# Kernel tuning notes

Measured on AMD Instinct MI355X. Metric: run time of the kernel, lower is better.

The kernel has to match this reference:

```python
import jax, jax.numpy as jnp
from jax import lax
import numpy as np

P, C, D, K, N = 16, 48, 32, 4, 262144
GRID = (512, 512, 128)
MAT_MODE = ((0, 1), (0, 2), (1, 2))


def setup_inputs() -> dict:
    key = jax.random.key(0)
    ks = jax.random.split(key, 9)
    pts = jax.random.uniform(ks[0], (1, N, 3), jnp.float32, -1.0, 1.0)
    topk_id = jax.random.randint(ks[1], (K,), 0, P)
    w = jax.random.uniform(ks[2], (K,), jnp.float32)
    topk_weight = w / jnp.sum(w)  # F.normalize(p=1)
    line0 = 0.1 * jax.random.normal(ks[3], (P, C, GRID[0]), jnp.float32)
    line1 = 0.1 * jax.random.normal(ks[4], (P, C, GRID[1]), jnp.float32)
    line2 = 0.1 * jax.random.normal(ks[5], (P, C, GRID[2]), jnp.float32)
    feat0 = 0.1 * jax.random.normal(ks[6], (P, C, D), jnp.float32)
    feat1 = 0.1 * jax.random.normal(ks[7], (P, C, D), jnp.float32)
    feat2 = 0.1 * jax.random.normal(ks[8], (P, C, D), jnp.float32)
    return dict(pts=pts, topk_id=topk_id, topk_weight=topk_weight,
                line0=line0, line1=line1, line2=line2,
                feat0=feat0, feat1=feat1, feat2=feat2)


def _interp_line(line, coords):
    # 1D linear interpolation (grid_sample with x=0, align_corners=True).
    # line: [K, C, G], coords: [n] in [-1, 1] -> [K, C, n]
    G = line.shape[-1]
    pos = (coords + 1.0) * 0.5 * (G - 1)
    i0 = jnp.clip(jnp.floor(pos), 0, G - 2).astype(jnp.int32)
    w = (pos - i0.astype(pos.dtype))  # [n]
    v0 = line[:, :, i0]       # gather -> [K, C, n]
    v1 = line[:, :, i0 + 1]
    return v0 * (1.0 - w) + v1 * w


def reference(pts, topk_id, topk_weight, line0, line1, line2, feat0, feat1, feat2):
    # pts is detached in the original (normalize_pts calls pts.detach())
    p = lax.stop_gradient(pts).reshape(-1, 3)  # [n, 3]
    lines = (line0[topk_id], line1[topk_id], line2[topk_id])   # [K, C, G_i]
    feats = (feat0[topk_id], feat1[topk_id], feat2[topk_id])   # [K, C, D]
    coord = [_interp_line(lines[i], p[:, i]) for i in range(3)]
    planes = [
        jnp.einsum('kcn,kcd->knd', coord[a] * coord[b], feats[i])
        for i, (a, b) in enumerate(MAT_MODE)
    ]
    pose_feats = jnp.concatenate(planes, axis=-1)           # [K, n, 3D]
    pose_feat = jnp.einsum('k,knd->nd', topk_weight, pose_feats)[None]  # [1, n, 96]
    return pose_feat
```

## Files before the change

### kernel.cpp

```cpp
#include <hip/hip_runtime.h>
#include <hip/hip_fp16.h>

typedef float f4 __attribute__((ext_vector_type(4)));
typedef float f32x4 __attribute__((ext_vector_type(4)));
typedef _Float16 f16x8 __attribute__((ext_vector_type(8)));
typedef unsigned int u32x4 __attribute__((ext_vector_type(4)));

#define NPTS 262144
#define CDIM 48
#define DDIM 32
#define KDIM 4
#define G0 512
#define G1 512
#define G2 128

#define TPB_TILES 4

#define T0_OFF 18432
#define T1_OFF (18432 + 98304)
#define T2_OFF (18432 + 2 * 98304)

static __forceinline__ __device__ unsigned short f2h(float f) {
    _Float16 h = (_Float16)f;
    return __builtin_bit_cast(unsigned short, h);
}
static __forceinline__ __device__ __half2 h2(unsigned int u) {
    return __builtin_bit_cast(__half2, u);
}
static __forceinline__ __device__ unsigned int h2u(__half2 h) {
    return __builtin_bit_cast(unsigned int, h);
}

__global__ void pack_kernel(const int* __restrict__ topk_id,
                            const float* __restrict__ tw,
                            const float* __restrict__ line0,
                            const float* __restrict__ line1,
                            const float* __restrict__ line2,
                            const float* __restrict__ feat0,
                            const float* __restrict__ feat1,
                            const float* __restrict__ feat2,
                            unsigned short* __restrict__ ws) {
    int tid = blockIdx.x * blockDim.x + threadIdx.x;
    int stride = gridDim.x * blockDim.x;

    for (int idx = tid; idx < 3 * 2 * 6 * 64 * 8; idx += stride) {
        int j = idx & 7;
        int l = (idx >> 3) & 63;
        int kt = (idx >> 9) % 6;
        int t = (idx / 3072) % 2;
        int i = idx / 6144;
        int kc = kt * 32 + (l >> 4) * 8 + j;
        int k = kc / 48;
        int c = kc - k * 48;
        int d = t * 16 + (l & 15);
        const float* f = (i == 0) ? feat0 : (i == 1) ? feat1 : feat2;
        float val = tw[k] * f[((size_t)topk_id[k] * CDIM + c) * DDIM + d];
        ws[idx] = f2h(val);
    }
    for (int idx = tid; idx < KDIM * G0 * CDIM; idx += stride) {
        int c = idx % CDIM;
        int g = (idx / CDIM) % G0;
        int k = idx / (CDIM * G0);
        int src = (topk_id[k] * CDIM + c) * G0 + g;
        ws[T0_OFF + idx] = f2h(line0[src]);
        ws[T1_OFF + idx] = f2h(line1[src]);
    }
    for (int idx = tid; idx < KDIM * G2 * CDIM; idx += stride) {
        int c = idx % CDIM;
        int g = (idx / CDIM) % G2;
        int k = idx / (CDIM * G2);
        ws[T2_OFF + idx] = f2h(line2[(topk_id[k] * CDIM + c) * G2 + g]);
    }
}

__global__ __launch_bounds__(256, 2) void main_kernel(const float* __restrict__ pts,
                                                      const unsigned short* __restrict__ ws,
                                                      float* __restrict__ out) {
    __shared__ __align__(16) unsigned short sWB[18432];

    const int lane = threadIdx.x & 63;
    const int wave = threadIdx.x >> 6;
    const int row = lane & 15;
    const int h = lane >> 4;

    float P0x, P0y, P0z, P1x, P1y, P1z, P2x, P2y, P2z, P3x, P3y, P3z;
    {
        const int pb = blockIdx.x * TPB_TILES * 64 + wave * 16 + row;
        P0x = pts[(pb + 0 * 64) * 3 + 0]; P0y = pts[(pb + 0 * 64) * 3 + 1]; P0z = pts[(pb + 0 * 64) * 3 + 2];
        P1x = pts[(pb + 1 * 64) * 3 + 0]; P1y = pts[(pb + 1 * 64) * 3 + 1]; P1z = pts[(pb + 1 * 64) * 3 + 2];
        P2x = pts[(pb + 2 * 64) * 3 + 0]; P2y = pts[(pb + 2 * 64) * 3 + 1]; P2z = pts[(pb + 2 * 64) * 3 + 2];
        P3x = pts[(pb + 3 * 64) * 3 + 0]; P3y = pts[(pb + 3 * 64) * 3 + 1]; P3z = pts[(pb + 3 * 64) * 3 + 2];
    }
    asm volatile("" : "+v"(P0x), "+v"(P0y), "+v"(P0z), "+v"(P1x), "+v"(P1y), "+v"(P1z),
                      "+v"(P2x), "+v"(P2y), "+v"(P2z), "+v"(P3x), "+v"(P3y), "+v"(P3z));

    {
        const u32x4* src = (const u32x4*)ws;
        u32x4* dst = (u32x4*)sWB;
        for (int i = threadIdx.x; i < 2304; i += 256) dst[i] = src[i];
    }
    __syncthreads();

    const unsigned short* T0 = ws + T0_OFF;
    const unsigned short* T1 = ws + T1_OFF;
    const unsigned short* T2 = ws + T2_OFF;
    const u32x4* wb = (const u32x4*)sWB;

#pragma unroll
    for (int tile = 0; tile < TPB_TILES; ++tile) {
        const int base = (blockIdx.x * TPB_TILES + tile) * 64 + wave * 16;

        const float px = (tile == 0) ? P0x : (tile == 1) ? P1x : (tile == 2) ? P2x : P3x;
        const float py = (tile == 0) ? P0y : (tile == 1) ? P1y : (tile == 2) ? P2y : P3y;
        const float pz = (tile == 0) ? P0z : (tile == 1) ? P1z : (tile == 2) ? P2z : P3z;

        float pos0 = (px + 1.0f) * (0.5f * (float)(G0 - 1));
        int i00 = min(max((int)floorf(pos0), 0), G0 - 2);
        float w0 = pos0 - (float)i00;

        float pos1 = (py + 1.0f) * (0.5f * (float)(G1 - 1));
        int i01 = min(max((int)floorf(pos1), 0), G1 - 2);
        float w1 = pos1 - (float)i01;

        float pos2 = (pz + 1.0f) * (0.5f * (float)(G2 - 1));
        int i02 = min(max((int)floorf(pos2), 0), G2 - 2);
        float w2 = pos2 - (float)i02;

        const __half2 W0 = __float2half2_rn(w0), OM0 = __float2half2_rn(1.0f - w0);
        const __half2 W1 = __float2half2_rn(w1), OM1 = __float2half2_rn(1.0f - w1);
        const __half2 W2 = __float2half2_rn(w2), OM2 = __float2half2_rn(1.0f - w2);

        f32x4 acc00 = {0.f, 0.f, 0.f, 0.f}, acc01 = acc00;
        f32x4 acc10 = acc00, acc11 = acc00;
        f32x4 acc20 = acc00, acc21 = acc00;

#define DECL_LD(n) u32x4 n##a0, n##b0, n##a1, n##b1, n##a2, n##b2
#define LOADKT(n, KT) {                                                        \
        int kc_ = (KT) * 32 + h * 8;                                           \
        int k_ = kc_ / 48;                                                     \
        int c_ = kc_ - k_ * 48;                                                \
        const unsigned short* t0_ = T0 + (k_ * G0 + i00) * CDIM + c_;          \
        const unsigned short* t1_ = T1 + (k_ * G1 + i01) * CDIM + c_;          \
        const unsigned short* t2_ = T2 + (k_ * G2 + i02) * CDIM + c_;          \
        n##a0 = *(const u32x4*)t0_;  n##b0 = *(const u32x4*)(t0_ + CDIM);      \
        n##a1 = *(const u32x4*)t1_;  n##b1 = *(const u32x4*)(t1_ + CDIM);      \
        n##a2 = *(const u32x4*)t2_;  n##b2 = *(const u32x4*)(t2_ + CDIM); }
#define KEEP36()                                                               \
    asm volatile("" : "+v"(q0a0), "+v"(q0b0), "+v"(q0a1), "+v"(q0b1),          \
                      "+v"(q0a2), "+v"(q0b2),                                  \
                      "+v"(q1a0), "+v"(q1b0), "+v"(q1a1), "+v"(q1b1),          \
                      "+v"(q1a2), "+v"(q1b2),                                  \
                      "+v"(q2a0), "+v"(q2b0), "+v"(q2a1), "+v"(q2b1),          \
                      "+v"(q2a2), "+v"(q2b2),                                  \
                      "+v"(q3a0), "+v"(q3b0), "+v"(q3a1), "+v"(q3b1),          \
                      "+v"(q3a2), "+v"(q3b2),                                  \
                      "+v"(q4a0), "+v"(q4b0), "+v"(q4a1), "+v"(q4b1),          \
                      "+v"(q4a2), "+v"(q4b2),                                  \
                      "+v"(q5a0), "+v"(q5b0), "+v"(q5a1), "+v"(q5b1),          \
                      "+v"(q5a2), "+v"(q5b2))
#define COMPUTEKT(n, KT) {                                                     \
        u32x4 pa01, pa02, pa12;                                                \
        _Pragma("unroll")                                                      \
        for (int j = 0; j < 4; ++j) {                                          \
            __half2 x0 = __hfma2(h2(n##b0[j]), W0, __hmul2(h2(n##a0[j]), OM0));\
            __half2 x1 = __hfma2(h2(n##b1[j]), W1, __hmul2(h2(n##a1[j]), OM1));\
            __half2 x2 = __hfma2(h2(n##b2[j]), W2, __hmul2(h2(n##a2[j]), OM2));\
            pa01[j] = h2u(__hmul2(x0, x1));                                    \
            pa02[j] = h2u(__hmul2(x0, x2));                                    \
            pa12[j] = h2u(__hmul2(x1, x2));                                    \
        }                                                                      \
        f16x8 fa01 = __builtin_bit_cast(f16x8, pa01);                          \
        f16x8 fa02 = __builtin_bit_cast(f16x8, pa02);                          \
        f16x8 fa12 = __builtin_bit_cast(f16x8, pa12);                          \
        acc00 = __builtin_amdgcn_mfma_f32_16x16x32_f16(__builtin_bit_cast(f16x8, wb[(0 * 6 + (KT)) * 64 + lane]), fa01, acc00, 0, 0, 0); \
        acc01 = __builtin_amdgcn_mfma_f32_16x16x32_f16(__builtin_bit_cast(f16x8, wb[(1 * 6 + (KT)) * 64 + lane]), fa01, acc01, 0, 0, 0); \
        acc10 = __builtin_amdgcn_mfma_f32_16x16x32_f16(__builtin_bit_cast(f16x8, wb[(2 * 6 + (KT)) * 64 + lane]), fa02, acc10, 0, 0, 0); \
        acc11 = __builtin_amdgcn_mfma_f32_16x16x32_f16(__builtin_bit_cast(f16x8, wb[(3 * 6 + (KT)) * 64 + lane]), fa02, acc11, 0, 0, 0); \
        acc20 = __builtin_amdgcn_mfma_f32_16x16x32_f16(__builtin_bit_cast(f16x8, wb[(4 * 6 + (KT)) * 64 + lane]), fa12, acc20, 0, 0, 0); \
        acc21 = __builtin_amdgcn_mfma_f32_16x16x32_f16(__builtin_bit_cast(f16x8, wb[(5 * 6 + (KT)) * 64 + lane]), fa12, acc21, 0, 0, 0); }

        DECL_LD(q0); DECL_LD(q1); DECL_LD(q2);
        DECL_LD(q3); DECL_LD(q4); DECL_LD(q5);

        LOADKT(q0, 0); LOADKT(q1, 1); LOADKT(q2, 2);
        LOADKT(q3, 3); LOADKT(q4, 4); LOADKT(q5, 5);
        KEEP36();

        COMPUTEKT(q0, 0);
        COMPUTEKT(q1, 1);
        COMPUTEKT(q2, 2);
        COMPUTEKT(q3, 3);
        COMPUTEKT(q4, 4);
        COMPUTEKT(q5, 5);

#undef DECL_LD
#undef LOADKT
#undef KEEP36
#undef COMPUTEKT

        {
            float* o = out + (size_t)(base + row) * 96 + h * 4;
            *(f4*)(o + 0)  = acc00;
            *(f4*)(o + 16) = acc01;
            *(f4*)(o + 32) = acc10;
            *(f4*)(o + 48) = acc11;
            *(f4*)(o + 64) = acc20;
            *(f4*)(o + 80) = acc21;
        }
    }
}

extern "C" void kernel_launch(void* const* d_in, const int* in_sizes, int n_in,
                              void* d_out, int out_size, void* d_ws, size_t ws_size,
                              hipStream_t stream) {
    const float* pts = (const float*)d_in[0];
    const int* topk_id = (const int*)d_in[1];
    const float* tw = (const float*)d_in[2];
    const float* line0 = (const float*)d_in[3];
    const float* line1 = (const float*)d_in[4];
    const float* line2 = (const float*)d_in[5];
    const float* feat0 = (const float*)d_in[6];
    const float* feat1 = (const float*)d_in[7];
    const float* feat2 = (const float*)d_in[8];
    float* out = (float*)d_out;
    unsigned short* ws = (unsigned short*)d_ws;

    pack_kernel<<<512, 256, 0, stream>>>(topk_id, tw, line0, line1, line2,
                                         feat0, feat1, feat2, ws);
    main_kernel<<<NPTS / (64 * TPB_TILES), 256, 0, stream>>>(pts, ws, out);
}
```

Baseline: 70.23 us.

## Sort points by z/x grid cell via counting sort to improve gather locality

Adds histogram, single-block scan, and scatter kernels that build a permutation grouping points by their (z-cell, x-cell) bucket, then has the main kernel process points in that order and write outputs scattered back to original indices. The aim is better cache locality for the line-table gathers, whose rows are scattered across random coordinates. In exchange it adds three extra launches, global atomics on a 65536-entry counter array, a serial single-block scan, an indirect point load, and non-contiguous output stores.

```diff
diff --git a/kernel.cpp b/kernel.cpp
--- a/kernel.cpp
+++ b/kernel.cpp
@@ -19,6 +19,10 @@
 #define T0_OFF 18432
 #define T1_OFF (18432 + 98304)
 #define T2_OFF (18432 + 2 * 98304)
+#define PERM_OFF 119808
+#define RANK_OFF 381952
+#define CNT_OFF 644096
+#define NBUCKET 65536
 
 static __forceinline__ __device__ unsigned short f2h(float f) {
     _Float16 h = (_Float16)f;
@@ -29,6 +33,14 @@
 }
 static __forceinline__ __device__ unsigned int h2u(__half2 h) {
     return __builtin_bit_cast(unsigned int, h);
+}
+static __forceinline__ __device__ int cell0(float x) {
+    float pos = (x + 1.0f) * (0.5f * (float)(G0 - 1));
+    return min(max((int)floorf(pos), 0), G0 - 2);
+}
+static __forceinline__ __device__ int cell2(float z) {
+    float pos = (z + 1.0f) * (0.5f * (float)(G2 - 1));
+    return min(max((int)floorf(pos), 0), G2 - 2);
 }
 
 __global__ void pack_kernel(const int* __restrict__ topk_id,
@@ -42,6 +54,9 @@
                             unsigned short* __restrict__ ws) {
     int tid = blockIdx.x * blockDim.x + threadIdx.x;
     int stride = gridDim.x * blockDim.x;
+    unsigned int* cnt = (unsigned int*)ws + CNT_OFF;
+
+    for (int idx = tid; idx < NBUCKET; idx += stride) cnt[idx] = 0;
 
     for (int idx = tid; idx < 3 * 2 * 6 * 64 * 8; idx += stride) {
         int j = idx & 7;
@@ -54,8 +69,7 @@
         int c = kc - k * 48;
         int d = t * 16 + (l & 15);
         const float* f = (i == 0) ? feat0 : (i == 1) ? feat1 : feat2;
-        float val = tw[k] * f[((size_t)topk_id[k] * CDIM + c) * DDIM + d];
-        ws[idx] = f2h(val);
+        ws[idx] = f2h(tw[k] * f[((size_t)topk_id[k] * CDIM + c) * DDIM + d]);
     }
     for (int idx = tid; idx < KDIM * G0 * CDIM; idx += stride) {
         int c = idx % CDIM;
@@ -73,6 +87,47 @@
     }
 }
 
+__global__ void hist_kernel(const float* __restrict__ pts, unsigned int* __restrict__ wsu) {
+    int n = blockIdx.x * blockDim.x + threadIdx.x;
+    if (n >= NPTS) return;
+    int key = (cell2(pts[n * 3 + 2]) << 9) | cell0(pts[n * 3 + 0]);
+    wsu[RANK_OFF + n] = atomicAdd(&wsu[CNT_OFF + key], 1u);
+}
+
+__global__ void scan_kernel(unsigned int* __restrict__ wsu) {
+    __shared__ unsigned int sa[1024], sb[1024];
+    unsigned int* counts = wsu + CNT_OFF;
+    int t = threadIdx.x;
+    unsigned int s = 0;
+    for (int i = 0; i < 64; ++i) s += counts[t * 64 + i];
+    sa[t] = s;
+    __syncthreads();
+    unsigned int* src = sa;
+    unsigned int* dst = sb;
+    for (int off = 1; off < 1024; off <<= 1) {
+        unsigned int v = src[t];
+        if (t >= off) v += src[t - off];
+        __syncthreads();
+        dst[t] = v;
+        __syncthreads();
+        unsigned int* tmp = src; src = dst; dst = tmp;
+    }
+    unsigned int run = (t == 0) ? 0u : src[t - 1];
+    for (int i = 0; i < 64; ++i) {
+        unsigned int c = counts[t * 64 + i];
+        counts[t * 64 + i] = run;
+        run += c;
+    }
+}
+
+__global__ void scatter_kernel(const float* __restrict__ pts, unsigned int* __restrict__ wsu) {
+    int n = blockIdx.x * blockDim.x + threadIdx.x;
+    if (n >= NPTS) return;
+    int key = (cell2(pts[n * 3 + 2]) << 9) | cell0(pts[n * 3 + 0]);
+    unsigned int slot = wsu[CNT_OFF + key] + wsu[RANK_OFF + n];
+    wsu[PERM_OFF + slot] = (unsigned int)n;
+}
+
 __global__ __launch_bounds__(256, 2) void main_kernel(const float* __restrict__ pts,
                                                       const unsigned short* __restrict__ ws,
                                                       float* __restrict__ out) {
@@ -82,14 +137,20 @@
     const int wave = threadIdx.x >> 6;
     const int row = lane & 15;
     const int h = lane >> 4;
-
+    const unsigned int* perm = (const unsigned int*)ws + PERM_OFF;
+
+    int n0, n1, n2, n3;
     float P0x, P0y, P0z, P1x, P1y, P1z, P2x, P2y, P2z, P3x, P3y, P3z;
     {
-        const int pb = blockIdx.x * TPB_TILES * 64 + wave * 16 + row;
-        P0x = pts[(pb + 0 * 64) * 3 + 0]; P0y = pts[(pb + 0 * 64) * 3 + 1]; P0z = pts[(pb + 0 * 64) * 3 + 2];
-        P1x = pts[(pb + 1 * 64) * 3 + 0]; P1y = pts[(pb + 1 * 64) * 3 + 1]; P1z = pts[(pb + 1 * 64) * 3 + 2];
-        P2x = pts[(pb + 2 * 64) * 3 + 0]; P2y = pts[(pb + 2 * 64) * 3 + 1]; P2z = pts[(pb + 2 * 64) * 3 + 2];
-        P3x = pts[(pb + 3 * 64) * 3 + 0]; P3y = pts[(pb + 3 * 64) * 3 + 1]; P3z = pts[(pb + 3 * 64) * 3 + 2];
+        const int sb = blockIdx.x * TPB_TILES * 64 + wave * 16 + row;
+        n0 = (int)perm[sb + 0 * 64];
+        n1 = (int)perm[sb + 1 * 64];
+        n2 = (int)perm[sb + 2 * 64];
+        n3 = (int)perm[sb + 3 * 64];
+        P0x = pts[n0 * 3 + 0]; P0y = pts[n0 * 3 + 1]; P0z = pts[n0 * 3 + 2];
+        P1x = pts[n1 * 3 + 0]; P1y = pts[n1 * 3 + 1]; P1z = pts[n1 * 3 + 2];
+        P2x = pts[n2 * 3 + 0]; P2y = pts[n2 * 3 + 1]; P2z = pts[n2 * 3 + 2];
+        P3x = pts[n3 * 3 + 0]; P3y = pts[n3 * 3 + 1]; P3z = pts[n3 * 3 + 2];
     }
     asm volatile("" : "+v"(P0x), "+v"(P0y), "+v"(P0z), "+v"(P1x), "+v"(P1y), "+v"(P1z),
                       "+v"(P2x), "+v"(P2y), "+v"(P2z), "+v"(P3x), "+v"(P3y), "+v"(P3z));
@@ -108,8 +169,7 @@
 
 #pragma unroll
     for (int tile = 0; tile < TPB_TILES; ++tile) {
-        const int base = (blockIdx.x * TPB_TILES + tile) * 64 + wave * 16;
-
+        const int nn = (tile == 0) ? n0 : (tile == 1) ? n1 : (tile == 2) ? n2 : n3;
         const float px = (tile == 0) ? P0x : (tile == 1) ? P1x : (tile == 2) ? P2x : P3x;
         const float py = (tile == 0) ? P0y : (tile == 1) ? P1y : (tile == 2) ? P2y : P3y;
         const float pz = (tile == 0) ? P0z : (tile == 1) ? P1z : (tile == 2) ? P2z : P3z;
@@ -199,7 +259,7 @@
 #undef COMPUTEKT
 
         {
-            float* o = out + (size_t)(base + row) * 96 + h * 4;
+            float* o = out + (size_t)nn * 96 + h * 4;
             *(f4*)(o + 0)  = acc00;
             *(f4*)(o + 16) = acc01;
             *(f4*)(o + 32) = acc10;
@@ -224,8 +284,12 @@
     const float* feat2 = (const float*)d_in[8];
     float* out = (float*)d_out;
     unsigned short* ws = (unsigned short*)d_ws;
+    unsigned int* wsu = (unsigned int*)d_ws;
 
     pack_kernel<<<512, 256, 0, stream>>>(topk_id, tw, line0, line1, line2,
                                          feat0, feat1, feat2, ws);
-    main_kernel<<<NPTS / (64 * TPB_TILES), 256, 0, stream>>>(pts, ws, out);
-}
+    hist_kernel<<<NPTS / 256, 256, 0, stream>>>(pts, wsu);
+    scan_kernel<<<1, 1024, 0, stream>>>(wsu);
+    scatter_kernel<<<NPTS / 256, 256, 0, stream>>>(pts, wsu);
+    main_kernel<<<NPTS / 256, 256, 0, stream>>>(pts, ws, out);
+}
```

After: 106.4 us. +51.4%, slower.

## Double-buffer per-tile gather loads across tiles and overlap with LDS weight staging

Applied to the files above, without the earlier changes.

Restructures the per-block tile loop into a software pipeline with two register sets (q and r). The next tile's 36 gathered table vectors are issued before the current tile's MFMA compute, and the first tile's loads go out before the shared-memory weight copy and barrier. Sched barriers pin this order. The aim is to hide global-load latency behind compute and the LDS fill. The cost is roughly double the load registers, which risks spills or lower occupancy under launch_bounds(256,2).

```diff
diff --git a/kernel.cpp b/kernel.cpp
--- a/kernel.cpp
+++ b/kernel.cpp
@@ -13,8 +13,6 @@
 #define G0 512
 #define G1 512
 #define G2 128
-
-#define TPB_TILES 4
 
 #define T0_OFF 18432
 #define T1_OFF (18432 + 98304)
@@ -54,8 +52,7 @@
         int c = kc - k * 48;
         int d = t * 16 + (l & 15);
         const float* f = (i == 0) ? feat0 : (i == 1) ? feat1 : feat2;
-        float val = tw[k] * f[((size_t)topk_id[k] * CDIM + c) * DDIM + d];
-        ws[idx] = f2h(val);
+        ws[idx] = f2h(tw[k] * f[((size_t)topk_id[k] * CDIM + c) * DDIM + d]);
     }
     for (int idx = tid; idx < KDIM * G0 * CDIM; idx += stride) {
         int c = idx % CDIM;
@@ -82,10 +79,11 @@
     const int wave = threadIdx.x >> 6;
     const int row = lane & 15;
     const int h = lane >> 4;
+    const int blkbase = blockIdx.x * 256 + wave * 16;
 
     float P0x, P0y, P0z, P1x, P1y, P1z, P2x, P2y, P2z, P3x, P3y, P3z;
     {
-        const int pb = blockIdx.x * TPB_TILES * 64 + wave * 16 + row;
+        const int pb = blkbase + row;
         P0x = pts[(pb + 0 * 64) * 3 + 0]; P0y = pts[(pb + 0 * 64) * 3 + 1]; P0z = pts[(pb + 0 * 64) * 3 + 2];
         P1x = pts[(pb + 1 * 64) * 3 + 0]; P1y = pts[(pb + 1 * 64) * 3 + 1]; P1z = pts[(pb + 1 * 64) * 3 + 2];
         P2x = pts[(pb + 2 * 64) * 3 + 0]; P2y = pts[(pb + 2 * 64) * 3 + 1]; P2z = pts[(pb + 2 * 64) * 3 + 2];
@@ -94,70 +92,54 @@
     asm volatile("" : "+v"(P0x), "+v"(P0y), "+v"(P0z), "+v"(P1x), "+v"(P1y), "+v"(P1z),
                       "+v"(P2x), "+v"(P2y), "+v"(P2z), "+v"(P3x), "+v"(P3y), "+v"(P3z));
 
-    {
-        const u32x4* src = (const u32x4*)ws;
-        u32x4* dst = (u32x4*)sWB;
-        for (int i = threadIdx.x; i < 2304; i += 256) dst[i] = src[i];
-    }
-    __syncthreads();
+#define PREP(t, PX, PY, PZ)                                                    \
+    float pos0_##t = (PX + 1.0f) * (0.5f * (float)(G0 - 1));                   \
+    int i00_##t = min(max((int)floorf(pos0_##t), 0), G0 - 2);                  \
+    float w0_##t = pos0_##t - (float)i00_##t;                                  \
+    float pos1_##t = (PY + 1.0f) * (0.5f * (float)(G1 - 1));                   \
+    int i01_##t = min(max((int)floorf(pos1_##t), 0), G1 - 2);                  \
+    float w1_##t = pos1_##t - (float)i01_##t;                                  \
+    float pos2_##t = (PZ + 1.0f) * (0.5f * (float)(G2 - 1));                   \
+    int i02_##t = min(max((int)floorf(pos2_##t), 0), G2 - 2);                  \
+    float w2_##t = pos2_##t - (float)i02_##t;
+
+    PREP(0, P0x, P0y, P0z)
+    PREP(1, P1x, P1y, P1z)
+    PREP(2, P2x, P2y, P2z)
+    PREP(3, P3x, P3y, P3z)
 
     const unsigned short* T0 = ws + T0_OFF;
     const unsigned short* T1 = ws + T1_OFF;
     const unsigned short* T2 = ws + T2_OFF;
-    const u32x4* wb = (const u32x4*)sWB;
-
-#pragma unroll
-    for (int tile = 0; tile < TPB_TILES; ++tile) {
-        const int base = (blockIdx.x * TPB_TILES + tile) * 64 + wave * 16;
-
-        const float px = (tile == 0) ? P0x : (tile == 1) ? P1x : (tile == 2) ? P2x : P3x;
-        const float py = (tile == 0) ? P0y : (tile == 1) ? P1y : (tile == 2) ? P2y : P3y;
-        const float pz = (tile == 0) ? P0z : (tile == 1) ? P1z : (tile == 2) ? P2z : P3z;
-
-        float pos0 = (px + 1.0f) * (0.5f * (float)(G0 - 1));
-        int i00 = min(max((int)floorf(pos0), 0), G0 - 2);
-        float w0 = pos0 - (float)i00;
-
-        float pos1 = (py + 1.0f) * (0.5f * (float)(G1 - 1));
-        int i01 = min(max((int)floorf(pos1), 0), G1 - 2);
-        float w1 = pos1 - (float)i01;
-
-        float pos2 = (pz + 1.0f) * (0.5f * (float)(G2 - 1));
-        int i02 = min(max((int)floorf(pos2), 0), G2 - 2);
-        float w2 = pos2 - (float)i02;
-
-        const __half2 W0 = __float2half2_rn(w0), OM0 = __float2half2_rn(1.0f - w0);
-        const __half2 W1 = __float2half2_rn(w1), OM1 = __float2half2_rn(1.0f - w1);
-        const __half2 W2 = __float2half2_rn(w2), OM2 = __float2half2_rn(1.0f - w2);
-
-        f32x4 acc00 = {0.f, 0.f, 0.f, 0.f}, acc01 = acc00;
-        f32x4 acc10 = acc00, acc11 = acc00;
-        f32x4 acc20 = acc00, acc21 = acc00;
 
 #define DECL_LD(n) u32x4 n##a0, n##b0, n##a1, n##b1, n##a2, n##b2
-#define LOADKT(n, KT) {                                                        \
+#define DECLW(w) DECL_LD(w##0); DECL_LD(w##1); DECL_LD(w##2); \
+                 DECL_LD(w##3); DECL_LD(w##4); DECL_LD(w##5)
+#define LOADKT(n, KT, t) {                                                     \
         int kc_ = (KT) * 32 + h * 8;                                           \
         int k_ = kc_ / 48;                                                     \
         int c_ = kc_ - k_ * 48;                                                \
-        const unsigned short* t0_ = T0 + (k_ * G0 + i00) * CDIM + c_;          \
-        const unsigned short* t1_ = T1 + (k_ * G1 + i01) * CDIM + c_;          \
-        const unsigned short* t2_ = T2 + (k_ * G2 + i02) * CDIM + c_;          \
+        const unsigned short* t0_ = T0 + (k_ * G0 + i00_##t) * CDIM + c_;      \
+        const unsigned short* t1_ = T1 + (k_ * G1 + i01_##t) * CDIM + c_;      \
+        const unsigned short* t2_ = T2 + (k_ * G2 + i02_##t) * CDIM + c_;      \
         n##a0 = *(const u32x4*)t0_;  n##b0 = *(const u32x4*)(t0_ + CDIM);      \
         n##a1 = *(const u32x4*)t1_;  n##b1 = *(const u32x4*)(t1_ + CDIM);      \
         n##a2 = *(const u32x4*)t2_;  n##b2 = *(const u32x4*)(t2_ + CDIM); }
-#define KEEP36()                                                               \
-    asm volatile("" : "+v"(q0a0), "+v"(q0b0), "+v"(q0a1), "+v"(q0b1),          \
-                      "+v"(q0a2), "+v"(q0b2),                                  \
-                      "+v"(q1a0), "+v"(q1b0), "+v"(q1a1), "+v"(q1b1),          \
-                      "+v"(q1a2), "+v"(q1b2),                                  \
-                      "+v"(q2a0), "+v"(q2b0), "+v"(q2a1), "+v"(q2b1),          \
-                      "+v"(q2a2), "+v"(q2b2),                                  \
-                      "+v"(q3a0), "+v"(q3b0), "+v"(q3a1), "+v"(q3b1),          \
-                      "+v"(q3a2), "+v"(q3b2),                                  \
-                      "+v"(q4a0), "+v"(q4b0), "+v"(q4a1), "+v"(q4b1),          \
-                      "+v"(q4a2), "+v"(q4b2),                                  \
-                      "+v"(q5a0), "+v"(q5b0), "+v"(q5a1), "+v"(q5b1),          \
-                      "+v"(q5a2), "+v"(q5b2))
+#define LOAD36(w, t) LOADKT(w##0, 0, t) LOADKT(w##1, 1, t) LOADKT(w##2, 2, t) \
+                     LOADKT(w##3, 3, t) LOADKT(w##4, 4, t) LOADKT(w##5, 5, t)
+#define KEEP36W(p)                                                             \
+    asm volatile("" : "+v"(p##0a0), "+v"(p##0b0), "+v"(p##0a1), "+v"(p##0b1),  \
+                      "+v"(p##0a2), "+v"(p##0b2),                              \
+                      "+v"(p##1a0), "+v"(p##1b0), "+v"(p##1a1), "+v"(p##1b1),  \
+                      "+v"(p##1a2), "+v"(p##1b2),                              \
+                      "+v"(p##2a0), "+v"(p##2b0), "+v"(p##2a1), "+v"(p##2b1),  \
+                      "+v"(p##2a2), "+v"(p##2b2),                              \
+                      "+v"(p##3a0), "+v"(p##3b0), "+v"(p##3a1), "+v"(p##3b1),  \
+                      "+v"(p##3a2), "+v"(p##3b2),                              \
+                      "+v"(p##4a0), "+v"(p##4b0), "+v"(p##4a1), "+v"(p##4b1),  \
+                      "+v"(p##4a2), "+v"(p##4b2),                              \
+                      "+v"(p##5a0), "+v"(p##5b0), "+v"(p##5a1), "+v"(p##5b1),  \
+                      "+v"(p##5a2), "+v"(p##5b2))
 #define COMPUTEKT(n, KT) {                                                     \
         u32x4 pa01, pa02, pa12;                                                \
         _Pragma("unroll")                                                      \
@@ -178,36 +160,62 @@
         acc11 = __builtin_amdgcn_mfma_f32_16x16x32_f16(__builtin_bit_cast(f16x8, wb[(3 * 6 + (KT)) * 64 + lane]), fa02, acc11, 0, 0, 0); \
         acc20 = __builtin_amdgcn_mfma_f32_16x16x32_f16(__builtin_bit_cast(f16x8, wb[(4 * 6 + (KT)) * 64 + lane]), fa12, acc20, 0, 0, 0); \
         acc21 = __builtin_amdgcn_mfma_f32_16x16x32_f16(__builtin_bit_cast(f16x8, wb[(5 * 6 + (KT)) * 64 + lane]), fa12, acc21, 0, 0, 0); }
-
-        DECL_LD(q0); DECL_LD(q1); DECL_LD(q2);
-        DECL_LD(q3); DECL_LD(q4); DECL_LD(q5);
-
-        LOADKT(q0, 0); LOADKT(q1, 1); LOADKT(q2, 2);
-        LOADKT(q3, 3); LOADKT(q4, 4); LOADKT(q5, 5);
-        KEEP36();
-
-        COMPUTEKT(q0, 0);
-        COMPUTEKT(q1, 1);
-        COMPUTEKT(q2, 2);
-        COMPUTEKT(q3, 3);
-        COMPUTEKT(q4, 4);
-        COMPUTEKT(q5, 5);
-
+#define COMPUTE_TILE(w, t) {                                                   \
+        const __half2 W0 = __float2half2_rn(w0_##t), OM0 = __float2half2_rn(1.0f - w0_##t); \
+        const __half2 W1 = __float2half2_rn(w1_##t), OM1 = __float2half2_rn(1.0f - w1_##t); \
+        const __half2 W2 = __float2half2_rn(w2_##t), OM2 = __float2half2_rn(1.0f - w2_##t); \
+        f32x4 acc00 = {0.f, 0.f, 0.f, 0.f}, acc01 = acc00;                     \
+        f32x4 acc10 = acc00, acc11 = acc00;                                    \
+        f32x4 acc20 = acc00, acc21 = acc00;                                    \
+        COMPUTEKT(w##0, 0) COMPUTEKT(w##1, 1) COMPUTEKT(w##2, 2)               \
+        COMPUTEKT(w##3, 3) COMPUTEKT(w##4, 4) COMPUTEKT(w##5, 5)               \
+        float* o = out + (size_t)(blkbase + (t) * 64 + row) * 96 + h * 4;      \
+        *(f4*)(o + 0)  = acc00;                                                \
+        *(f4*)(o + 16) = acc01;                                                \
+        *(f4*)(o + 32) = acc10;                                                \
+        *(f4*)(o + 48) = acc11;                                                \
+        *(f4*)(o + 64) = acc20;                                                \
+        *(f4*)(o + 80) = acc21; }
+
+    DECLW(q); DECLW(r);
+
+    LOAD36(q, 0)
+
+    {
+        const u32x4* src = (const u32x4*)ws;
+        u32x4* dst = (u32x4*)sWB;
+        for (int i = threadIdx.x; i < 2304; i += 256) dst[i] = src[i];
+    }
+    __syncthreads();
+
+    const u32x4* wb = (const u32x4*)sWB;
+
+    LOAD36(r, 1)
+    __builtin_amdgcn_sched_barrier(0);
+    KEEP36W(q);
+    COMPUTE_TILE(q, 0)
+
+    LOAD36(q, 2)
+    __builtin_amdgcn_sched_barrier(0);
+    KEEP36W(r);
+    COMPUTE_TILE(r, 1)
+
+    LOAD36(r, 3)
+    __builtin_amdgcn_sched_barrier(0);
+    KEEP36W(q);
+    COMPUTE_TILE(q, 2)
+
+    KEEP36W(r);
+    COMPUTE_TILE(r, 3)
+
+#undef PREP
 #undef DECL_LD
+#undef DECLW
 #undef LOADKT
-#undef KEEP36
+#undef LOAD36
+#undef KEEP36W
 #undef COMPUTEKT
-
-        {
-            float* o = out + (size_t)(base + row) * 96 + h * 4;
-            *(f4*)(o + 0)  = acc00;
-            *(f4*)(o + 16) = acc01;
-            *(f4*)(o + 32) = acc10;
-            *(f4*)(o + 48) = acc11;
-            *(f4*)(o + 64) = acc20;
-            *(f4*)(o + 80) = acc21;
-        }
-    }
+#undef COMPUTE_TILE
 }
 
 extern "C" void kernel_launch(void* const* d_in, const int* in_sizes, int n_in,
@@ -227,5 +235,5 @@
 
     pack_kernel<<<512, 256, 0, stream>>>(topk_id, tw, line0, line1, line2,
                                          feat0, feat1, feat2, ws);
-    main_kernel<<<NPTS / (64 * TPB_TILES), 256, 0, stream>>>(pts, ws, out);
-}
+    main_kernel<<<NPTS / 256, 256, 0, stream>>>(pts, ws, out);
+}
```

Result: slower. 154.2 us (+119.6%).
